# Kernel tuning notes

Measured on AMD Instinct MI355X. Metric: run time of the kernel, lower is better.

Reference implementation:

```python
import jax, jax.numpy as jnp
import numpy as np


def _box_iou(b1, b2):
    # torchvision.ops.box_iou: b1 [N,4], b2 [M,4] in (x1,y1,x2,y2) -> [N,M]
    area1 = (b1[:, 2] - b1[:, 0]) * (b1[:, 3] - b1[:, 1])
    area2 = (b2[:, 2] - b2[:, 0]) * (b2[:, 3] - b2[:, 1])
    lt = jnp.maximum(b1[:, None, :2], b2[None, :, :2])  # [N,M,2]
    rb = jnp.minimum(b1[:, None, 2:], b2[None, :, 2:])  # [N,M,2]
    wh = jnp.clip(rb - lt, 0.0)
    inter = wh[..., 0] * wh[..., 1]
    return inter / (area1[:, None] + area2[None, :] - inter)


def _hungarian_max(iou_np):
    # Maximize total IoU == minimize -IoU. iou_np: [N_pred, M_tgt], N >= M.
    # Classic O(n^2 m) shortest-augmenting-path Hungarian (host-side numpy;
    # the assignment is combinatorial and produces integer indices only).
    cost = -np.asarray(iou_np, dtype=np.float64).T  # [n=M_tgt, m=N_pred], n <= m
    n, m = cost.shape
    INF = 1e18
    u = np.zeros(n + 1)
    v = np.zeros(m + 1)
    p = np.zeros(m + 1, dtype=np.int64)   # p[j] = 1-based row matched to col j
    way = np.zeros(m + 1, dtype=np.int64)
    for i in range(1, n + 1):
        p[0] = i
        j0 = 0
        minv = np.full(m + 1, INF)
        used = np.zeros(m + 1, dtype=bool)
        while True:
            used[j0] = True
            i0 = p[j0]
            free = ~used[1:]
            cur = cost[i0 - 1, :] - u[i0] - v[1:]
            upd = free & (cur < minv[1:])
            mv = minv[1:]
            wy = way[1:]
            mv[upd] = cur[upd]
            wy[upd] = j0
            masked = np.where(free, mv, INF)
            j1 = int(np.argmin(masked)) + 1
            delta = masked[j1 - 1]
            u[p[used]] += delta
            v[used] -= delta
            mv[free] -= delta
            j0 = j1
            if p[j0] == 0:
                break
        while j0 != 0:
            j1 = way[j0]
            p[j0] = p[j1]
            j0 = j1
    row4col = p[1:]
    cols = np.nonzero(row4col > 0)[0]          # matched pred indices
    rows = row4col[cols] - 1                   # matched target indices
    return cols.astype(np.int64), rows.astype(np.int64)  # (matched_pred, matched_target)


def _make_boxes(kc, ks, shape):
    c = jax.random.uniform(kc, shape + (2,), dtype=jnp.float32)
    s = jax.random.uniform(ks, shape + (2,), dtype=jnp.float32) * 0.2 + 0.01
    return jnp.concatenate([c - s / 2, c + s / 2], axis=-1)


def setup_inputs() -> dict:
    key = jax.random.key(0)
    k1, k2, k3, k4, k5, k6 = jax.random.split(key, 6)
    N, C, B, K = 100000, 81, 16, 8
    result_boxes = _make_boxes(k1, k2, (N,))                      # [N,4] valid boxes
    result_confs = jax.random.normal(k3, (N, C), dtype=jnp.float32)
    target_locs = _make_boxes(k4, k5, (B, K))                     # [B,K,4]
    target_labels = jax.random.randint(k6, (B, K), 0, C, dtype=jnp.int64)
    return {
        "result_boxes": result_boxes,
        "result_confs": result_confs,
        "target_locs": target_locs,
        "target_labels": target_labels,
    }


def reference(result_boxes, result_confs, target_locs, target_labels):
    # Concatenating per-image targets == flattening batch dim
    total_locs = target_locs.reshape(-1, 4)        # [M,4]
    total_labels = target_labels.reshape(-1)       # [M]

    iou = _box_iou(result_boxes, total_locs)       # [N,M]
    matched_pred, matched_target = _hungarian_max(iou)
    mp = jnp.asarray(matched_pred)
    mt = jnp.asarray(matched_target)

    # SmoothL1 (beta=1, reduction='mean' over the 4 coords), summed over pairs
    d = result_boxes[mp] - total_locs[mt]          # [M,4]
    ad = jnp.abs(d)
    sl1 = jnp.where(ad < 1.0, 0.5 * d * d, ad - 0.5)
    reg_loss = jnp.sum(jnp.mean(sl1, axis=-1))

    # CrossEntropy per single (unbatched) sample, summed over pairs
    logits = result_confs[mp]                      # [M,C]
    labels = total_labels[mt]                      # [M]
    logp = jax.nn.log_softmax(logits, axis=-1)
    cls_loss = -jnp.sum(jnp.take_along_axis(logp, labels[:, None], axis=-1))

    train_acc = jnp.sum((jnp.argmax(logits, axis=-1) == labels).astype(jnp.int64))
    return (reg_loss + cls_loss, train_acc)
```

## Files before the change

kernel.cpp:

```cpp
#include <hip/hip_runtime.h>
#include <cstdint>
#include <cstddef>

typedef unsigned long long u64;
typedef unsigned int u32;

#define SLICES 2
#define SCAND 192
#define CAND 384
#define NSLOT 6
#define NBINS 4096
#define SEL_THR 1024
#define SEL_TARGET 128
#define POOLCAP 4096
#define MASKW 3200
#define TOP8 8

__device__ __forceinline__ float iou_f32(float4 p, float4 t, float area_t) {
  float area1 = (p.z - p.x) * (p.w - p.y);
  float ltx = fmaxf(p.x, t.x);
  float lty = fmaxf(p.y, t.y);
  float rbx = fminf(p.z, t.z);
  float rby = fminf(p.w, t.w);
  float wx = fmaxf(rbx - ltx, 0.0f);
  float wy = fmaxf(rby - lty, 0.0f);
  float inter = wx * wy;
  return inter / (area1 + area_t - inter);
}

__device__ __forceinline__ u64 map_cost(double cur) {
  u64 b = (u64)__double_as_longlong(cur);
  if (b == 0x8000000000000000ull) b = 0;
  return (b >> 63) ? ~b : (b | 0x8000000000000000ull);
}
__device__ __forceinline__ double unmap_cost(u64 m) {
  u64 b = (m >> 63) ? (m ^ 0x8000000000000000ull) : ~m;
  return __longlong_as_double((long long)b);
}


__global__ __launch_bounds__(SEL_THR) void select_kernel(const float4* __restrict__ pbox,
                                                         const float4* __restrict__ tbox,
                                                         u64* __restrict__ ckey,
                                                         int M, int NROWS) {
  __shared__ u32 s_hist[NBINS];
  __shared__ int s_csum[SEL_THR];
  __shared__ u64 s_pool[POOLCAP];
  __shared__ int s_n, s_n2, s_B;
  const int tid = threadIdx.x;
  const int lane = tid & 63;
  const int slice = blockIdx.x, row = blockIdx.y;
  const int sw = (M + SLICES - 1) / SLICES;
  const int base = slice * sw;
  const int send = min(base + sw, M);
  const float4 tb = tbox[row];
  const float area_t = (tb.z - tb.x) * (tb.w - tb.y);
  u64* orow_key = ckey + (size_t)row * CAND + slice * SCAND;

  for (int b = tid; b < NBINS; b += SEL_THR) s_hist[b] = 0;
  if (tid == 0) { s_n = 0; s_n2 = 0; s_B = 0; }
  __syncthreads();

  const u64 lowmask = (1ull << lane) - 1ull;
  const int iters = (sw + SEL_THR - 1) / SEL_THR;
  for (int it = 0; it < iters; ++it) {
    int j = base + it * SEL_THR + tid;
    bool inr = (j < send);
    float io = -1.0f;
    if (inr) io = iou_f32(pbox[j], tb, area_t);
    bool pos = inr && (io > 0.0f);
    u64 pm = __ballot(pos);
    int wn = (int)__popcll(pm);
    if (wn) {
      int wb = 0;
      if (lane == 0) wb = atomicAdd(&s_n, wn);
      wb = __shfl(wb, 0);
      if (pos) {
        int idx = wb + (int)__popcll(pm & lowmask);
        if (idx < POOLCAP) s_pool[idx] = ((u64)__float_as_uint(io) << 32) | (u64)(0xFFFFFFFFu - (u32)j);
        atomicAdd(&s_hist[__float_as_uint(io) >> 18], 1u);
      }
    }
  }
  __syncthreads();
  const int np = s_n;

  {
    int b0 = tid * 4;
    s_csum[tid] = (int)(s_hist[b0] + s_hist[b0 + 1] + s_hist[b0 + 2] + s_hist[b0 + 3]);
  }
  __syncthreads();

  if (tid < 64) {
    if (np >= SEL_TARGET) {
      int R = 0; bool found = false;
      for (int ch = SEL_THR / 64 - 1; ch >= 0 && !found; --ch) {
        int cum = s_csum[ch * 64 + tid];
        for (int off = 1; off < 64; off <<= 1) {
          int o = __shfl_down(cum, off);
          if (tid + off < 64) cum += o;
        }
        int chunksum = __shfl(cum, 0);
        if (R + chunksum >= SEL_TARGET) {
          u64 m = __ballot(R + cum >= SEL_TARGET);
          int l = 63 - __clzll(m);
          int R2 = R + ((l < 63) ? __shfl(cum, l + 1) : 0);
          if (tid == 0) {
            int bb = (ch * 64 + l) * 4;
            int B2 = bb;
            for (int b = bb + 3; b >= bb; --b) {
              R2 += (int)s_hist[b];
              if (R2 >= SEL_TARGET) { B2 = b; break; }
            }
            s_B = B2;
          }
          found = true;
        } else R += chunksum;
      }
    }
  }
  __syncthreads();
  const int B = s_B;

  if (np >= SEL_TARGET) {
    if (np <= POOLCAP) {
      for (int t = tid; t < np; t += SEL_THR) {
        u64 k = s_pool[t];
        if ((u32)(k >> 50) >= (u32)B) {
          int pos = atomicAdd(&s_n2, 1);
          if (pos < SCAND) orow_key[pos] = k;
        }
      }
    } else {
      for (int j = base + tid; j < send; j += SEL_THR) {
        float io = iou_f32(pbox[j], tb, area_t);
        if (io > 0.0f && (int)(__float_as_uint(io) >> 18) >= B) {
          int pos = atomicAdd(&s_n2, 1);
          if (pos < SCAND) orow_key[pos] = ((u64)__float_as_uint(io) << 32) | (u64)(0xFFFFFFFFu - (u32)j);
        }
      }
    }
    __syncthreads();
  } else {
    for (int t = tid; t < np; t += SEL_THR) {
      u64 k = s_pool[t];
      int pos = atomicAdd(&s_n2, 1);
      if (pos < SCAND) orow_key[pos] = k;
    }
    __syncthreads();
    if (tid < 64) {
      int need = SEL_TARGET - np, got = 0;
      int base_n = s_n2;
      for (int b2 = base; b2 < send && got < need; b2 += 64) {
        int j = b2 + tid;
        float io = (j < send) ? iou_f32(pbox[j], tb, area_t) : -1.0f;
        bool z = (j < send) && (io == 0.0f);
        u64 zm = __ballot(z);
        int rank = (int)__popcll(zm & ((1ull << tid) - 1ull));
        if (z && rank < need - got) {
          int pos = base_n + got + rank;
          if (pos < SCAND) orow_key[pos] = (u64)(0xFFFFFFFFu - (u32)j);
        }
        int zn = (int)__popcll(zm); if (zn > need - got) zn = need - got;
        got += zn;
      }
      if (tid == 0) s_n2 = base_n + got;
    }
    __syncthreads();
  }
  int n = min(s_n2, SCAND);
  for (int t2 = n + tid; t2 < SCAND; t2 += SEL_THR) orow_key[t2] = 0ull;
}

#define DPP_STEP(CTRL) do { \
  u32 ohi = (u32)__builtin_amdgcn_update_dpp((int)0xFFFFFFFF, (int)khi, (CTRL), 0xF, 0xF, false); \
  u32 olo = (u32)__builtin_amdgcn_update_dpp((int)0xFFFFFFFF, (int)klo, (CTRL), 0xF, 0xF, false); \
  int ocl =      __builtin_amdgcn_update_dpp((int)0x7FFFFFFF, kcol,     (CTRL), 0xF, 0xF, false); \
  bool lt = (ohi < khi) || (ohi == khi && ((olo < klo) || (olo == klo && ocl < kcol))); \
  if (lt) { khi = ohi; klo = olo; kcol = ocl; } \
} while (0)

#define DPPMAX(CTRL) do { \
  u32 oh2 = (u32)__builtin_amdgcn_update_dpp(0, (int)mhi, (CTRL), 0xF, 0xF, false); \
  u32 ol2 = (u32)__builtin_amdgcn_update_dpp(0, (int)mlo, (CTRL), 0xF, 0xF, false); \
  bool gt = (oh2 > mhi) || (oh2 == mhi && ol2 > mlo); \
  if (gt) { mhi = oh2; mlo = ol2; } \
} while (0)

__global__ __launch_bounds__(64) void top8_kernel(const u64* __restrict__ ckey,
                                                  u64* __restrict__ top8g, int NROWS) {
  const int lane = threadIdx.x;
  const int row = blockIdx.x;
  const u64* kp = ckey + (size_t)row * CAND;
  u64 k[NSLOT];
#pragma unroll
  for (int s = 0; s < NSLOT; ++s) k[s] = kp[(s << 6) + lane];
  u64 out = 0;
  for (int r = 0; r < TOP8; ++r) {
    u64 lmax = 0;
#pragma unroll
    for (int s = 0; s < NSLOT; ++s) if (k[s] > lmax) lmax = k[s];
    u32 mhi = (u32)(lmax >> 32), mlo = (u32)lmax;
    DPPMAX(0x111); DPPMAX(0x112); DPPMAX(0x114); DPPMAX(0x118); DPPMAX(0x142); DPPMAX(0x143);
    u32 ghi = (u32)__builtin_amdgcn_readlane((int)mhi, 63);
    u32 glo = (u32)__builtin_amdgcn_readlane((int)mlo, 63);
    u64 g = ((u64)ghi << 32) | (u64)glo;
    if (lane == r) out = g;
#pragma unroll
    for (int s = 0; s < NSLOT; ++s) if (k[s] == g) k[s] = 0;
  }
  if (lane < TOP8) top8g[(size_t)row * TOP8 + lane] = out;
}

#define STAGE_EVAL(KARR) do { \
  u64 lmax = 0; \
  _Pragma("unroll") \
  for (int s = 0; s < NSLOT; ++s) { \
    u64 k = (KARR)[s]; \
    if (k) { \
      u32 cw = 0xFFFFFFFFu - (u32)k; \
      if ((s_mask[cw >> 5] >> (cw & 31u)) & 1u) k = 0; \
      if (k > lmax) lmax = k; \
    } \
  } \
  u32 mhi = (u32)(lmax >> 32), mlo = (u32)lmax; \
  DPPMAX(0x111); DPPMAX(0x112); DPPMAX(0x114); DPPMAX(0x118); DPPMAX(0x142); DPPMAX(0x143); \
  u32 ghi = (u32)__builtin_amdgcn_readlane((int)mhi, 63); \
  u32 glo = (u32)__builtin_amdgcn_readlane((int)mlo, 63); \
  head_key = ((u64)ghi << 32) | (u64)glo; \
} while (0)

#define STAGE_LDS(RR) do { \
  u64 k = 0; \
  if (lane < TOP8) { \
    k = s_top8[(RR) - 1][lane]; \
    u32 cw = 0xFFFFFFFFu - (u32)k; \
    if ((s_mask[cw >> 5] >> (cw & 31u)) & 1u) k = 0; \
  } \
  u32 mhi = (u32)(k >> 32), mlo = (u32)k; \
  DPPMAX(0x111); DPPMAX(0x112); DPPMAX(0x114); \
  u32 ghi = (u32)__builtin_amdgcn_readlane((int)mhi, 7); \
  u32 glo = (u32)__builtin_amdgcn_readlane((int)mlo, 7); \
  head_key = ((u64)ghi << 32) | (u64)glo; \
  if (head_key == 0) { \
    u64 ck[NSLOT]; \
    const u64* kp = ckey + (size_t)((RR) - 1) * CAND; \
    _Pragma("unroll") \
    for (int s = 0; s < NSLOT; ++s) ck[s] = kp[(s << 6) + lane]; \
    STAGE_EVAL(ck); \
  } \
} while (0)

#define RECOMP_IOU(I0) do { \
  float4 tbi = s_tb[(I0) - 1]; \
  float ati = s_ta[(I0) - 1]; \
  oi0 = iou_f32(ob0, tbi, ati); \
  oi1 = iou_f32(ob1, tbi, ati); \
} while (0)

__global__ __launch_bounds__(64, 1) void match_kernel(const float4* __restrict__ pbox,
                                                      const float4* __restrict__ tboxg,
                                                      const u64* __restrict__ ckey,
                                                      const u64* __restrict__ top8g,
                                                      int* __restrict__ pairs,
                                                      int M, int NROWS) {
  const int lane = threadIdx.x;
  __shared__ u32 s_mask[MASKW];
  __shared__ u64 s_top8[128][TOP8];
  __shared__ float4 s_tb[128];
  __shared__ float  s_ta[128];

  for (int i = lane; i < MASKW; i += 64) s_mask[i] = 0;
  for (int i = lane; i < NROWS; i += 64) {
    float4 t = tboxg[i];
    s_tb[i] = t;
    s_ta[i] = (t.z - t.x) * (t.w - t.y);
  }
  for (int i = lane; i < NROWS * TOP8; i += 64) s_top8[i >> 3][i & 7] = top8g[i];
  __syncthreads();

  float4 zf = make_float4(0.f, 0.f, 0.f, 0.f);
  double u_a = 0.0, u_b = 0.0;
  int f_a = 0, f_b = 0;
  int oc0 = -1, orow0 = 0, ovis0 = 0; double ov0 = 0.0; float4 ob0 = zf; float oi0 = 0.0f;
  int oc1 = -1, orow1 = 0, ovis1 = 0; double ov1 = 0.0; float4 ob1 = zf; float oi1 = 0.0f;
  int nown = 0;

  u64 head_key = 0;
  float4 hbox = zf;
  int row = 1, i0 = 1;
  double u_i0 = 0.0;

  STAGE_LDS(1);
  hbox = pbox[0xFFFFFFFFu - (u32)head_key];
  f_a = (lane == 0); f_b = 0;
  u_i0 = 0.0;

  for (int guard = 0; guard < 5000; ++guard) {
    if (head_key == 0) break;

    u32 bhi = 0xFFFFFFFFu, blo = 0xFFFFFFFFu; int bcol = 0x7fffffff; int bsl = 15;
    if (oc0 >= 0 && ovis0 != row) {
      double cur = ((-(double)oi0) - u_i0) - ov0;
      u64 mk = map_cost(cur);
      bhi = (u32)(mk >> 32); blo = (u32)mk; bcol = oc0; bsl = 6;
    }
    if (oc1 >= 0 && ovis1 != row) {
      double cur = ((-(double)oi1) - u_i0) - ov1;
      u64 mk = map_cost(cur);
      u32 hi = (u32)(mk >> 32), lo = (u32)mk;
      bool t = (hi < bhi) || (hi == bhi && ((lo < blo) || (lo == blo && oc1 < bcol)));
      if (t) { bhi = hi; blo = lo; bcol = oc1; bsl = 7; }
    }
    u32 khi = bhi, klo = blo; int kcol = bcol;
    DPP_STEP(0x111); DPP_STEP(0x112); DPP_STEP(0x114); DPP_STEP(0x118);
    DPP_STEP(0x142); DPP_STEP(0x143);
    u32 rhi = (u32)__builtin_amdgcn_readlane((int)khi, 63);
    u32 rlo = (u32)__builtin_amdgcn_readlane((int)klo, 63);
    int rcol = __builtin_amdgcn_readlane(kcol, 63);

    float hio = __uint_as_float((u32)(head_key >> 32));
    int hcol = (int)(0xFFFFFFFFu - (u32)head_key);
    double curh = (-(double)hio) - u_i0;
    u64 mh = map_cost(curh);
    u32 hhi = (u32)(mh >> 32), hlo = (u32)mh;
    bool head_wins = (hhi < rhi) || (hhi == rhi && ((hlo < rlo) || (hlo == rlo && hcol < rcol)));
    const double delta = unmap_cost(head_wins ? mh : (((u64)rhi << 32) | (u64)rlo));

    if (f_a) u_a += delta;
    if (f_b) u_b += delta;
    u_i0 += delta;
    if (oc0 >= 0 && ovis0 == row) ov0 -= delta;
    if (oc1 >= 0 && ovis1 == row) ov1 -= delta;

    if (head_wins) {
      if (lane == 0) {
        pairs[row - 1] = hcol;
        atomicOr(&s_mask[(u32)hcol >> 5], 1u << ((u32)hcol & 31u));
      }
      int ne = nown, nl = ne & 63, nh = ne >> 6;
      if (lane == nl) {
        if (nh == 0) { oc0 = hcol; orow0 = row; ovis0 = 0; ov0 = 0.0; ob0 = hbox; }
        else         { oc1 = hcol; orow1 = row; ovis1 = 0; ov1 = 0.0; ob1 = hbox; }
      }
      nown = ne + 1;
      if (row == NROWS) break;
      ++row; i0 = row;
      asm volatile("s_waitcnt lgkmcnt(0)" ::: "memory");
      STAGE_LDS(row);
      hbox = pbox[0xFFFFFFFFu - (u32)head_key];
      RECOMP_IOU(row);
      f_a = (lane == ((row - 1) & 63)) && (((row - 1) >> 6) == 0);
      f_b = (lane == ((row - 1) & 63)) && (((row - 1) >> 6) == 1);
      u_i0 = 0.0;
    } else {
      bool eq = (bhi == rhi) && (blo == rlo) && (bcol == rcol);
      u64 wm = __ballot(eq);
      int L = (int)__ffsll((long long)wm) - 1;
      L = __builtin_amdgcn_readfirstlane(L);
      int s_w = __builtin_amdgcn_readlane(bsl, L);
      int o = __builtin_amdgcn_readlane((s_w == 6) ? orow0 : orow1, L);
      o = __builtin_amdgcn_readfirstlane(o);
      if (lane == L) { if (s_w == 6) ovis0 = row; else ovis1 = row; }
      int ol = (o - 1) & 63, oh = (o - 1) >> 6;
      if (lane == ol) { if (oh == 0) f_a = 1; else f_b = 1; }
      double uo = oh ? u_b : u_a;
      int uhi2 = __builtin_amdgcn_readlane(__double2hiint(uo), ol);
      int ulo2 = __builtin_amdgcn_readlane(__double2loint(uo), ol);
      u_i0 = __hiloint2double(uhi2, ulo2);
      i0 = o;
      STAGE_LDS(o);
      hbox = pbox[0xFFFFFFFFu - (u32)head_key];
      RECOMP_IOU(o);
    }
  }
}

__global__ __launch_bounds__(256) void loss_kernel(const float4* __restrict__ pbox,
                                                   const float* __restrict__ confs,
                                                   const float4* __restrict__ tbox,
                                                   const int* __restrict__ tlab,
                                                   const int* __restrict__ pairs,
                                                   float* __restrict__ out,
                                                   int NROWS, int C) {
  const int tid = threadIdx.x;
  __shared__ float s_reg[256];
  __shared__ float s_cls[256];
  __shared__ int   s_acc[256];
  float reg = 0.0f, cls = 0.0f; int acc = 0;
  if (tid < NROWS) {
    int pred = pairs[tid];
    float4 pb = pbox[pred];
    float4 tb = tbox[tid];
    float d0 = pb.x - tb.x, d1 = pb.y - tb.y, d2 = pb.z - tb.z, d3 = pb.w - tb.w;
    float a0 = fabsf(d0), a1 = fabsf(d1), a2 = fabsf(d2), a3 = fabsf(d3);
    float s = 0.0f;
    s += (a0 < 1.0f) ? 0.5f * d0 * d0 : a0 - 0.5f;
    s += (a1 < 1.0f) ? 0.5f * d1 * d1 : a1 - 0.5f;
    s += (a2 < 1.0f) ? 0.5f * d2 * d2 : a2 - 0.5f;
    s += (a3 < 1.0f) ? 0.5f * d3 * d3 : a3 - 0.5f;
    reg = s * 0.25f;

    const float* lg = confs + (long long)pred * C;
    float mx = lg[0]; int am = 0;
    for (int k = 1; k < C; ++k) { float x = lg[k]; if (x > mx) { mx = x; am = k; } }
    double se = 0.0;
    for (int k = 0; k < C; ++k) se += exp((double)(lg[k] - mx));
    int lab = tlab[tid];
    double logp = (double)(lg[lab] - mx) - log(se);
    cls = (float)(-logp);
    acc = (am == lab) ? 1 : 0;
  }
  s_reg[tid] = reg; s_cls[tid] = cls; s_acc[tid] = acc;
  __syncthreads();
  for (int s2 = 128; s2 > 0; s2 >>= 1) {
    if (tid < s2) {
      s_reg[tid] += s_reg[tid + s2];
      s_cls[tid] += s_cls[tid + s2];
      s_acc[tid] += s_acc[tid + s2];
    }
    __syncthreads();
  }
  if (tid == 0) {
    out[0] = s_reg[0] + s_cls[0];
    out[1] = (float)s_acc[0];
  }
}

extern "C" void kernel_launch(void* const* d_in, const int* in_sizes, int n_in,
                              void* d_out, int out_size, void* d_ws, size_t ws_size,
                              hipStream_t stream) {
  const float4* pbox  = (const float4*)d_in[0];
  const float*  confs = (const float*)d_in[1];
  const float4* tbox  = (const float4*)d_in[2];
  const int*    tlab  = (const int*)d_in[3];

  int N = in_sizes[0] / 4;
  int C = in_sizes[1] / N;
  int NROWS = in_sizes[2] / 4;
  int M = N;

  char* w = (char*)d_ws;
  auto alloc = [&](size_t sz) { char* r = w; w += (sz + 255) & ~(size_t)255; return r; };
  u64* ckey  = (u64*)alloc((size_t)NROWS * CAND * sizeof(u64));
  u64* top8g = (u64*)alloc((size_t)NROWS * TOP8 * sizeof(u64));
  int* pairs = (int*)alloc((size_t)(NROWS + 8) * sizeof(int));

  select_kernel<<<dim3(SLICES, NROWS), SEL_THR, 0, stream>>>(pbox, tbox, ckey, M, NROWS);
  top8_kernel<<<NROWS, 64, 0, stream>>>(ckey, top8g, NROWS);
  match_kernel<<<1, 64, 0, stream>>>(pbox, tbox, ckey, top8g, pairs, M, NROWS);
  loss_kernel<<<1, 256, 0, stream>>>(pbox, confs, tbox, tlab, pairs,
                                     (float*)d_out, NROWS, C);
}
```

Measured before the change: 251.2 us.

## Add fast-path bound check to skip owned-column scan and keep top8 in registers

The match loop keeps a running bound (vmax) on owned-column potentials. When the head candidate's reduced cost provably beats every owned column, it augments directly and skips the IoU recompute and the wave-wide DPP min-reduction. Per-row top-8 candidates and target boxes now live in registers, fetched with readlane and a select tree, instead of LDS. This trades LDS traffic and the per-step reduction for more register pressure and a correctness-critical bound argument.

Result: slower. 279.3 us (+11.2%).

```diff
diff --git a/kernel.cpp b/kernel.cpp
--- a/kernel.cpp
+++ b/kernel.cpp
@@ -212,51 +212,23 @@
   if (lane < TOP8) top8g[(size_t)row * TOP8 + lane] = out;
 }
 
-#define STAGE_EVAL(KARR) do { \
-  u64 lmax = 0; \
-  _Pragma("unroll") \
-  for (int s = 0; s < NSLOT; ++s) { \
-    u64 k = (KARR)[s]; \
-    if (k) { \
-      u32 cw = 0xFFFFFFFFu - (u32)k; \
-      if ((s_mask[cw >> 5] >> (cw & 31u)) & 1u) k = 0; \
-      if (k > lmax) lmax = k; \
-    } \
-  } \
-  u32 mhi = (u32)(lmax >> 32), mlo = (u32)lmax; \
-  DPPMAX(0x111); DPPMAX(0x112); DPPMAX(0x114); DPPMAX(0x118); DPPMAX(0x142); DPPMAX(0x143); \
-  u32 ghi = (u32)__builtin_amdgcn_readlane((int)mhi, 63); \
-  u32 glo = (u32)__builtin_amdgcn_readlane((int)mlo, 63); \
-  head_key = ((u64)ghi << 32) | (u64)glo; \
-} while (0)
-
-#define STAGE_LDS(RR) do { \
-  u64 k = 0; \
-  if (lane < TOP8) { \
-    k = s_top8[(RR) - 1][lane]; \
-    u32 cw = 0xFFFFFFFFu - (u32)k; \
-    if ((s_mask[cw >> 5] >> (cw & 31u)) & 1u) k = 0; \
-  } \
-  u32 mhi = (u32)(k >> 32), mlo = (u32)k; \
-  DPPMAX(0x111); DPPMAX(0x112); DPPMAX(0x114); \
-  u32 ghi = (u32)__builtin_amdgcn_readlane((int)mhi, 7); \
-  u32 glo = (u32)__builtin_amdgcn_readlane((int)mlo, 7); \
-  head_key = ((u64)ghi << 32) | (u64)glo; \
-  if (head_key == 0) { \
-    u64 ck[NSLOT]; \
-    const u64* kp = ckey + (size_t)((RR) - 1) * CAND; \
-    _Pragma("unroll") \
-    for (int s = 0; s < NSLOT; ++s) ck[s] = kp[(s << 6) + lane]; \
-    STAGE_EVAL(ck); \
-  } \
-} while (0)
-
-#define RECOMP_IOU(I0) do { \
-  float4 tbi = s_tb[(I0) - 1]; \
-  float ati = s_ta[(I0) - 1]; \
-  oi0 = iou_f32(ob0, tbi, ati); \
-  oi1 = iou_f32(ob1, tbi, ati); \
-} while (0)
+__device__ __forceinline__ u64 sel16(const u64* t8, int ri) {
+  u64 a0 = (ri & 1) ? t8[1]  : t8[0];
+  u64 a1 = (ri & 1) ? t8[3]  : t8[2];
+  u64 a2 = (ri & 1) ? t8[5]  : t8[4];
+  u64 a3 = (ri & 1) ? t8[7]  : t8[6];
+  u64 a4 = (ri & 1) ? t8[9]  : t8[8];
+  u64 a5 = (ri & 1) ? t8[11] : t8[10];
+  u64 a6 = (ri & 1) ? t8[13] : t8[12];
+  u64 a7 = (ri & 1) ? t8[15] : t8[14];
+  u64 b0 = (ri & 2) ? a1 : a0;
+  u64 b1 = (ri & 2) ? a3 : a2;
+  u64 b2 = (ri & 2) ? a5 : a4;
+  u64 b3 = (ri & 2) ? a7 : a6;
+  u64 c0 = (ri & 4) ? b1 : b0;
+  u64 c1 = (ri & 4) ? b3 : b2;
+  return (ri & 8) ? c1 : c0;
+}
 
 __global__ __launch_bounds__(64, 1) void match_kernel(const float4* __restrict__ pbox,
                                                       const float4* __restrict__ tboxg,
@@ -266,112 +238,190 @@
                                                       int M, int NROWS) {
   const int lane = threadIdx.x;
   __shared__ u32 s_mask[MASKW];
-  __shared__ u64 s_top8[128][TOP8];
-  __shared__ float4 s_tb[128];
-  __shared__ float  s_ta[128];
-
   for (int i = lane; i < MASKW; i += 64) s_mask[i] = 0;
-  for (int i = lane; i < NROWS; i += 64) {
-    float4 t = tboxg[i];
-    s_tb[i] = t;
-    s_ta[i] = (t.z - t.x) * (t.w - t.y);
-  }
-  for (int i = lane; i < NROWS * TOP8; i += 64) s_top8[i >> 3][i & 7] = top8g[i];
   __syncthreads();
 
   float4 zf = make_float4(0.f, 0.f, 0.f, 0.f);
+  float4 tbA = (lane < NROWS) ? tboxg[lane] : zf;
+  float4 tbB = (lane + 64 < NROWS) ? tboxg[lane + 64] : zf;
+
+  u64 t8[16];
+#pragma unroll
+  for (int r = 0; r < 16; ++r) {
+    int rw = (lane >> 3) + (r << 3);
+    t8[r] = (rw < NROWS) ? top8g[(size_t)rw * TOP8 + (lane & 7)] : 0ull;
+  }
+
   double u_a = 0.0, u_b = 0.0;
   int f_a = 0, f_b = 0;
-  int oc0 = -1, orow0 = 0, ovis0 = 0; double ov0 = 0.0; float4 ob0 = zf; float oi0 = 0.0f;
-  int oc1 = -1, orow1 = 0, ovis1 = 0; double ov1 = 0.0; float4 ob1 = zf; float oi1 = 0.0f;
+  int oc0 = -1, orow0 = 0, ovis0 = 0; double ov0 = 0.0; float4 ob0 = zf;
+  int oc1 = -1, orow1 = 0, ovis1 = 0; double ov1 = 0.0; float4 ob1 = zf;
   int nown = 0;
+  double vmax = 0.0;
+  bool inchain = false;
 
   u64 head_key = 0;
   float4 hbox = zf;
   int row = 1, i0 = 1;
   double u_i0 = 0.0;
 
-  STAGE_LDS(1);
+  auto stage_reg = [&](int rr) -> u64 {
+    int rr0 = rr - 1;
+    u64 sel = sel16(t8, rr0 >> 3);
+    int g = rr0 & 7;
+    if ((lane >> 3) != g) sel = 0;
+    u32 mhi = (u32)(sel >> 32), mlo = (u32)sel;
+    DPPMAX(0x111); DPPMAX(0x112); DPPMAX(0x114);
+    u32 ghi = (u32)__builtin_amdgcn_readlane((int)mhi, (g << 3) + 7);
+    u32 glo = (u32)__builtin_amdgcn_readlane((int)mlo, (g << 3) + 7);
+    u64 hk = ((u64)ghi << 32) | (u64)glo;
+    if (hk == 0) {
+      asm volatile("s_waitcnt lgkmcnt(0)" ::: "memory");
+      const u64* kp = ckey + (size_t)rr0 * CAND;
+      u64 lmax = 0;
+#pragma unroll
+      for (int s = 0; s < NSLOT; ++s) {
+        u64 k = kp[(s << 6) + lane];
+        if (k) {
+          u32 cw = 0xFFFFFFFFu - (u32)k;
+          if ((s_mask[cw >> 5] >> (cw & 31u)) & 1u) k = 0;
+          if (k > lmax) lmax = k;
+        }
+      }
+      u32 mh2 = (u32)(lmax >> 32), ml2 = (u32)lmax;
+      { u32 mhi = mh2, mlo = ml2;
+        DPPMAX(0x111); DPPMAX(0x112); DPPMAX(0x114); DPPMAX(0x118); DPPMAX(0x142); DPPMAX(0x143);
+        mh2 = (u32)__builtin_amdgcn_readlane((int)mhi, 63);
+        ml2 = (u32)__builtin_amdgcn_readlane((int)mlo, 63); }
+      hk = ((u64)mh2 << 32) | (u64)ml2;
+    }
+    return hk;
+  };
+
+  head_key = stage_reg(1);
   hbox = pbox[0xFFFFFFFFu - (u32)head_key];
   f_a = (lane == 0); f_b = 0;
   u_i0 = 0.0;
 
-  for (int guard = 0; guard < 5000; ++guard) {
+  bool fin = false;
+  for (int guard = 0; guard < 5000 && !fin; ++guard) {
     if (head_key == 0) break;
-
-    u32 bhi = 0xFFFFFFFFu, blo = 0xFFFFFFFFu; int bcol = 0x7fffffff; int bsl = 15;
-    if (oc0 >= 0 && ovis0 != row) {
-      double cur = ((-(double)oi0) - u_i0) - ov0;
-      u64 mk = map_cost(cur);
-      bhi = (u32)(mk >> 32); blo = (u32)mk; bcol = oc0; bsl = 6;
-    }
-    if (oc1 >= 0 && ovis1 != row) {
-      double cur = ((-(double)oi1) - u_i0) - ov1;
-      u64 mk = map_cost(cur);
-      u32 hi = (u32)(mk >> 32), lo = (u32)mk;
-      bool t = (hi < bhi) || (hi == bhi && ((lo < blo) || (lo == blo && oc1 < bcol)));
-      if (t) { bhi = hi; blo = lo; bcol = oc1; bsl = 7; }
-    }
-    u32 khi = bhi, klo = blo; int kcol = bcol;
-    DPP_STEP(0x111); DPP_STEP(0x112); DPP_STEP(0x114); DPP_STEP(0x118);
-    DPP_STEP(0x142); DPP_STEP(0x143);
-    u32 rhi = (u32)__builtin_amdgcn_readlane((int)khi, 63);
-    u32 rlo = (u32)__builtin_amdgcn_readlane((int)klo, 63);
-    int rcol = __builtin_amdgcn_readlane(kcol, 63);
 
     float hio = __uint_as_float((u32)(head_key >> 32));
     int hcol = (int)(0xFFFFFFFFu - (u32)head_key);
     double curh = (-(double)hio) - u_i0;
-    u64 mh = map_cost(curh);
-    u32 hhi = (u32)(mh >> 32), hlo = (u32)mh;
-    bool head_wins = (hhi < rhi) || (hhi == rhi && ((hlo < rlo) || (hlo == rlo && hcol < rcol)));
-    const double delta = unmap_cost(head_wins ? mh : (((u64)rhi << 32) | (u64)rlo));
+
+    bool fast;
+    if (nown == 0) fast = true;
+    else {
+      double bound = (-1.0 - u_i0) - vmax;
+      fast = (bound > curh);
+    }
+
+    double delta;
+    bool do_aug;
+    int jc = hcol;
+
+    if (fast) {
+      delta = curh;
+      do_aug = true;
+    } else {
+      int li = (i0 - 1) & 63, hb2 = (i0 - 1) >> 6;
+      float tx = __int_as_float(__builtin_amdgcn_readlane(__float_as_int(hb2 ? tbB.x : tbA.x), li));
+      float ty = __int_as_float(__builtin_amdgcn_readlane(__float_as_int(hb2 ? tbB.y : tbA.y), li));
+      float tz = __int_as_float(__builtin_amdgcn_readlane(__float_as_int(hb2 ? tbB.z : tbA.z), li));
+      float tw = __int_as_float(__builtin_amdgcn_readlane(__float_as_int(hb2 ? tbB.w : tbA.w), li));
+      float4 tbi = make_float4(tx, ty, tz, tw);
+      float ati = (tz - tx) * (tw - ty);
+
+      u32 bhi = 0xFFFFFFFFu, blo = 0xFFFFFFFFu; int bcol = 0x7fffffff; int bsl = 15;
+      if (oc0 >= 0 && ovis0 != row) {
+        float io2 = iou_f32(ob0, tbi, ati);
+        double cur = ((-(double)io2) - u_i0) - ov0;
+        u64 mk = map_cost(cur);
+        bhi = (u32)(mk >> 32); blo = (u32)mk; bcol = oc0; bsl = 6;
+      }
+      if (oc1 >= 0 && ovis1 != row) {
+        float io2 = iou_f32(ob1, tbi, ati);
+        double cur = ((-(double)io2) - u_i0) - ov1;
+        u64 mk = map_cost(cur);
+        u32 hi = (u32)(mk >> 32), lo = (u32)mk;
+        bool t = (hi < bhi) || (hi == bhi && ((lo < blo) || (lo == blo && oc1 < bcol)));
+        if (t) { bhi = hi; blo = lo; bcol = oc1; bsl = 7; }
+      }
+      u32 khi = bhi, klo = blo; int kcol = bcol;
+      DPP_STEP(0x111); DPP_STEP(0x112); DPP_STEP(0x114); DPP_STEP(0x118);
+      DPP_STEP(0x142); DPP_STEP(0x143);
+      u32 rhi = (u32)__builtin_amdgcn_readlane((int)khi, 63);
+      u32 rlo = (u32)__builtin_amdgcn_readlane((int)klo, 63);
+      int rcol = __builtin_amdgcn_readlane(kcol, 63);
+
+      u64 mh = map_cost(curh);
+      u32 hhi = (u32)(mh >> 32), hlo = (u32)mh;
+      bool head_wins = (hhi < rhi) || (hhi == rhi && ((hlo < rlo) || (hlo == rlo && hcol < rcol)));
+      delta = unmap_cost(head_wins ? mh : (((u64)rhi << 32) | (u64)rlo));
+      do_aug = head_wins;
+
+      if (!head_wins) {
+        bool eq = (bhi == rhi) && (blo == rlo) && (bcol == rcol);
+        u64 wm = __ballot(eq);
+        int L = (int)__ffsll((long long)wm) - 1;
+        L = __builtin_amdgcn_readfirstlane(L);
+        int s_w = __builtin_amdgcn_readlane(bsl, L);
+        int o = __builtin_amdgcn_readlane((s_w == 6) ? orow0 : orow1, L);
+        o = __builtin_amdgcn_readfirstlane(o);
+        if (f_a) u_a += delta;
+        if (f_b) u_b += delta;
+        u_i0 += delta;
+        if (oc0 >= 0 && ovis0 == row) ov0 -= delta;
+        if (oc1 >= 0 && ovis1 == row) ov1 -= delta;
+        if (inchain) vmax = fmax(vmax, vmax - delta);
+        inchain = true;
+        if (lane == L) { if (s_w == 6) ovis0 = row; else ovis1 = row; }
+        int ol = (o - 1) & 63, oh = (o - 1) >> 6;
+        if (lane == ol) { if (oh == 0) f_a = 1; else f_b = 1; }
+        double uo = oh ? u_b : u_a;
+        int uhi2 = __builtin_amdgcn_readlane(__double2hiint(uo), ol);
+        int ulo2 = __builtin_amdgcn_readlane(__double2loint(uo), ol);
+        u_i0 = __hiloint2double(uhi2, ulo2);
+        i0 = o;
+        head_key = stage_reg(o);
+        hbox = pbox[0xFFFFFFFFu - (u32)head_key];
+        continue;
+      }
+    }
 
     if (f_a) u_a += delta;
     if (f_b) u_b += delta;
-    u_i0 += delta;
     if (oc0 >= 0 && ovis0 == row) ov0 -= delta;
     if (oc1 >= 0 && ovis1 == row) ov1 -= delta;
-
-    if (head_wins) {
-      if (lane == 0) {
-        pairs[row - 1] = hcol;
-        atomicOr(&s_mask[(u32)hcol >> 5], 1u << ((u32)hcol & 31u));
-      }
+    if (inchain) vmax = fmax(vmax, vmax - delta);
+
+    if (lane == 0) {
+      pairs[row - 1] = jc;
+      atomicOr(&s_mask[(u32)jc >> 5], 1u << ((u32)jc & 31u));
+    }
+    {
+      u32 cjw = 0xFFFFFFFFu - (u32)jc;
+#pragma unroll
+      for (int r = 0; r < 16; ++r) if ((u32)t8[r] == cjw) t8[r] = 0;
+    }
+    {
       int ne = nown, nl = ne & 63, nh = ne >> 6;
       if (lane == nl) {
-        if (nh == 0) { oc0 = hcol; orow0 = row; ovis0 = 0; ov0 = 0.0; ob0 = hbox; }
-        else         { oc1 = hcol; orow1 = row; ovis1 = 0; ov1 = 0.0; ob1 = hbox; }
+        if (nh == 0) { oc0 = jc; orow0 = row; ovis0 = 0; ov0 = 0.0; ob0 = hbox; }
+        else         { oc1 = jc; orow1 = row; ovis1 = 0; ov1 = 0.0; ob1 = hbox; }
       }
       nown = ne + 1;
-      if (row == NROWS) break;
-      ++row; i0 = row;
-      asm volatile("s_waitcnt lgkmcnt(0)" ::: "memory");
-      STAGE_LDS(row);
-      hbox = pbox[0xFFFFFFFFu - (u32)head_key];
-      RECOMP_IOU(row);
+    }
+    vmax = fmax(vmax, 0.0);
+    if (row == NROWS) { fin = true; }
+    else {
+      ++row; i0 = row; u_i0 = 0.0; inchain = false;
       f_a = (lane == ((row - 1) & 63)) && (((row - 1) >> 6) == 0);
       f_b = (lane == ((row - 1) & 63)) && (((row - 1) >> 6) == 1);
-      u_i0 = 0.0;
-    } else {
-      bool eq = (bhi == rhi) && (blo == rlo) && (bcol == rcol);
-      u64 wm = __ballot(eq);
-      int L = (int)__ffsll((long long)wm) - 1;
-      L = __builtin_amdgcn_readfirstlane(L);
-      int s_w = __builtin_amdgcn_readlane(bsl, L);
-      int o = __builtin_amdgcn_readlane((s_w == 6) ? orow0 : orow1, L);
-      o = __builtin_amdgcn_readfirstlane(o);
-      if (lane == L) { if (s_w == 6) ovis0 = row; else ovis1 = row; }
-      int ol = (o - 1) & 63, oh = (o - 1) >> 6;
-      if (lane == ol) { if (oh == 0) f_a = 1; else f_b = 1; }
-      double uo = oh ? u_b : u_a;
-      int uhi2 = __builtin_amdgcn_readlane(__double2hiint(uo), ol);
-      int ulo2 = __builtin_amdgcn_readlane(__double2loint(uo), ol);
-      u_i0 = __hiloint2double(uhi2, ulo2);
-      i0 = o;
-      STAGE_LDS(o);
+      head_key = stage_reg(row);
       hbox = pbox[0xFFFFFFFFu - (u32)head_key];
-      RECOMP_IOU(o);
     }
   }
 }
```

## Fuse loss into match kernel and precompute top-8 boxes to shorten serial chain

Applied to the files above, without the earlier changes.

The top8 kernel now also gathers the prediction boxes for each row's top-8 candidates, so the serial Hungarian loop takes the head box from LDS via a lane readlane instead of a dependent global load. When a row finishes, the next row's head is taken from the top two candidates already prefetched, and IoU is recomputed on the fly from target boxes held in registers. The loss kernel is folded into the match kernel (256 threads, one wave runs the matching), which removes a launch and the global pairs buffer. This adds LDS and register pressure and makes the serial loop's control flow more complex.

After: 279.8 us. 1.11x slower.

```diff
diff --git a/kernel.cpp b/kernel.cpp
--- a/kernel.cpp
+++ b/kernel.cpp
@@ -187,8 +187,10 @@
   if (gt) { mhi = oh2; mlo = ol2; } \
 } while (0)
 
-__global__ __launch_bounds__(64) void top8_kernel(const u64* __restrict__ ckey,
-                                                  u64* __restrict__ top8g, int NROWS) {
+__global__ __launch_bounds__(64) void top8_kernel(const float4* __restrict__ pbox,
+                                                  const u64* __restrict__ ckey,
+                                                  u64* __restrict__ top8g,
+                                                  float4* __restrict__ top8b, int NROWS) {
   const int lane = threadIdx.x;
   const int row = blockIdx.x;
   const u64* kp = ckey + (size_t)row * CAND;
@@ -209,189 +211,221 @@
 #pragma unroll
     for (int s = 0; s < NSLOT; ++s) if (k[s] == g) k[s] = 0;
   }
-  if (lane < TOP8) top8g[(size_t)row * TOP8 + lane] = out;
-}
-
-#define STAGE_EVAL(KARR) do { \
-  u64 lmax = 0; \
-  _Pragma("unroll") \
-  for (int s = 0; s < NSLOT; ++s) { \
-    u64 k = (KARR)[s]; \
-    if (k) { \
-      u32 cw = 0xFFFFFFFFu - (u32)k; \
-      if ((s_mask[cw >> 5] >> (cw & 31u)) & 1u) k = 0; \
-      if (k > lmax) lmax = k; \
-    } \
+  if (lane < TOP8) {
+    top8g[(size_t)row * TOP8 + lane] = out;
+    int col = (int)(0xFFFFFFFFu - (u32)out);
+    top8b[(size_t)row * TOP8 + lane] = out ? pbox[col] : make_float4(0.f, 0.f, 0.f, 0.f);
+  }
+}
+
+#define RDLF(X, L) __int_as_float(__builtin_amdgcn_readlane(__float_as_int(X), (L)))
+
+#define COLD_STAGE(RR) do { \
+  u64 kk = 0; float4 kb = zf; \
+  if (lane < TOP8) { \
+    kk = s_t8[((RR) - 1) * TOP8 + lane]; \
+    kb = s_t8b[((RR) - 1) * TOP8 + lane]; \
+    u32 cw = 0xFFFFFFFFu - (u32)kk; \
+    if (kk && ((s_mask[cw >> 5] >> (cw & 31u)) & 1u)) kk = 0; \
   } \
-  u32 mhi = (u32)(lmax >> 32), mlo = (u32)lmax; \
-  DPPMAX(0x111); DPPMAX(0x112); DPPMAX(0x114); DPPMAX(0x118); DPPMAX(0x142); DPPMAX(0x143); \
-  u32 ghi = (u32)__builtin_amdgcn_readlane((int)mhi, 63); \
-  u32 glo = (u32)__builtin_amdgcn_readlane((int)mlo, 63); \
-  head_key = ((u64)ghi << 32) | (u64)glo; \
-} while (0)
-
-#define STAGE_LDS(RR) do { \
-  u64 k = 0; \
-  if (lane < TOP8) { \
-    k = s_top8[(RR) - 1][lane]; \
-    u32 cw = 0xFFFFFFFFu - (u32)k; \
-    if ((s_mask[cw >> 5] >> (cw & 31u)) & 1u) k = 0; \
-  } \
-  u32 mhi = (u32)(k >> 32), mlo = (u32)k; \
+  u32 mhi = (u32)(kk >> 32), mlo = (u32)kk; \
   DPPMAX(0x111); DPPMAX(0x112); DPPMAX(0x114); \
   u32 ghi = (u32)__builtin_amdgcn_readlane((int)mhi, 7); \
   u32 glo = (u32)__builtin_amdgcn_readlane((int)mlo, 7); \
   head_key = ((u64)ghi << 32) | (u64)glo; \
-  if (head_key == 0) { \
-    u64 ck[NSLOT]; \
-    const u64* kp = ckey + (size_t)((RR) - 1) * CAND; \
+  if (head_key != 0) { \
+    int eL = (int)__ffsll((long long)__ballot(kk == head_key && kk != 0)) - 1; \
+    eL = __builtin_amdgcn_readfirstlane(eL); \
+    hbox.x = RDLF(kb.x, eL); hbox.y = RDLF(kb.y, eL); \
+    hbox.z = RDLF(kb.z, eL); hbox.w = RDLF(kb.w, eL); \
+  } else { \
+    const u64* kp2 = ckey + (size_t)((RR) - 1) * CAND; \
+    u64 lmax = 0; \
     _Pragma("unroll") \
-    for (int s = 0; s < NSLOT; ++s) ck[s] = kp[(s << 6) + lane]; \
-    STAGE_EVAL(ck); \
+    for (int s = 0; s < NSLOT; ++s) { \
+      u64 kf = kp2[(s << 6) + lane]; \
+      if (kf) { \
+        u32 cw = 0xFFFFFFFFu - (u32)kf; \
+        if ((s_mask[cw >> 5] >> (cw & 31u)) & 1u) kf = 0; \
+        if (kf > lmax) lmax = kf; \
+      } \
+    } \
+    u32 m2hi = (u32)(lmax >> 32), m2lo = (u32)lmax; \
+    { u32 mhi = m2hi, mlo = m2lo; \
+      DPPMAX(0x111); DPPMAX(0x112); DPPMAX(0x114); DPPMAX(0x118); DPPMAX(0x142); DPPMAX(0x143); \
+      m2hi = (u32)__builtin_amdgcn_readlane((int)mhi, 63); \
+      m2lo = (u32)__builtin_amdgcn_readlane((int)mlo, 63); } \
+    head_key = ((u64)m2hi << 32) | (u64)m2lo; \
+    if (head_key) hbox = pbox[0xFFFFFFFFu - (u32)head_key]; \
   } \
 } while (0)
 
-#define RECOMP_IOU(I0) do { \
-  float4 tbi = s_tb[(I0) - 1]; \
-  float ati = s_ta[(I0) - 1]; \
-  oi0 = iou_f32(ob0, tbi, ati); \
-  oi1 = iou_f32(ob1, tbi, ati); \
-} while (0)
-
-__global__ __launch_bounds__(64, 1) void match_kernel(const float4* __restrict__ pbox,
-                                                      const float4* __restrict__ tboxg,
-                                                      const u64* __restrict__ ckey,
-                                                      const u64* __restrict__ top8g,
-                                                      int* __restrict__ pairs,
-                                                      int M, int NROWS) {
-  const int lane = threadIdx.x;
+__global__ __launch_bounds__(256, 1) void match_kernel(const float4* __restrict__ pbox,
+                                                       const float4* __restrict__ tboxg,
+                                                       const u64* __restrict__ ckey,
+                                                       const u64* __restrict__ top8g,
+                                                       const float4* __restrict__ top8b,
+                                                       const float* __restrict__ confs,
+                                                       const int* __restrict__ tlab,
+                                                       float* __restrict__ out,
+                                                       int M, int NROWS, int C) {
+  const int tid = threadIdx.x;
+  const int lane = tid & 63;
+  const int wv = tid >> 6;
   __shared__ u32 s_mask[MASKW];
-  __shared__ u64 s_top8[128][TOP8];
-  __shared__ float4 s_tb[128];
-  __shared__ float  s_ta[128];
-
-  for (int i = lane; i < MASKW; i += 64) s_mask[i] = 0;
-  for (int i = lane; i < NROWS; i += 64) {
-    float4 t = tboxg[i];
-    s_tb[i] = t;
-    s_ta[i] = (t.z - t.x) * (t.w - t.y);
-  }
-  for (int i = lane; i < NROWS * TOP8; i += 64) s_top8[i >> 3][i & 7] = top8g[i];
-  __syncthreads();
-
-  float4 zf = make_float4(0.f, 0.f, 0.f, 0.f);
-  double u_a = 0.0, u_b = 0.0;
-  int f_a = 0, f_b = 0;
-  int oc0 = -1, orow0 = 0, ovis0 = 0; double ov0 = 0.0; float4 ob0 = zf; float oi0 = 0.0f;
-  int oc1 = -1, orow1 = 0, ovis1 = 0; double ov1 = 0.0; float4 ob1 = zf; float oi1 = 0.0f;
-  int nown = 0;
-
-  u64 head_key = 0;
-  float4 hbox = zf;
-  int row = 1, i0 = 1;
-  double u_i0 = 0.0;
-
-  STAGE_LDS(1);
-  hbox = pbox[0xFFFFFFFFu - (u32)head_key];
-  f_a = (lane == 0); f_b = 0;
-  u_i0 = 0.0;
-
-  for (int guard = 0; guard < 5000; ++guard) {
-    if (head_key == 0) break;
-
-    u32 bhi = 0xFFFFFFFFu, blo = 0xFFFFFFFFu; int bcol = 0x7fffffff; int bsl = 15;
-    if (oc0 >= 0 && ovis0 != row) {
-      double cur = ((-(double)oi0) - u_i0) - ov0;
-      u64 mk = map_cost(cur);
-      bhi = (u32)(mk >> 32); blo = (u32)mk; bcol = oc0; bsl = 6;
-    }
-    if (oc1 >= 0 && ovis1 != row) {
-      double cur = ((-(double)oi1) - u_i0) - ov1;
-      u64 mk = map_cost(cur);
-      u32 hi = (u32)(mk >> 32), lo = (u32)mk;
-      bool t = (hi < bhi) || (hi == bhi && ((lo < blo) || (lo == blo && oc1 < bcol)));
-      if (t) { bhi = hi; blo = lo; bcol = oc1; bsl = 7; }
-    }
-    u32 khi = bhi, klo = blo; int kcol = bcol;
-    DPP_STEP(0x111); DPP_STEP(0x112); DPP_STEP(0x114); DPP_STEP(0x118);
-    DPP_STEP(0x142); DPP_STEP(0x143);
-    u32 rhi = (u32)__builtin_amdgcn_readlane((int)khi, 63);
-    u32 rlo = (u32)__builtin_amdgcn_readlane((int)klo, 63);
-    int rcol = __builtin_amdgcn_readlane(kcol, 63);
-
-    float hio = __uint_as_float((u32)(head_key >> 32));
-    int hcol = (int)(0xFFFFFFFFu - (u32)head_key);
-    double curh = (-(double)hio) - u_i0;
-    u64 mh = map_cost(curh);
-    u32 hhi = (u32)(mh >> 32), hlo = (u32)mh;
-    bool head_wins = (hhi < rhi) || (hhi == rhi && ((hlo < rlo) || (hlo == rlo && hcol < rcol)));
-    const double delta = unmap_cost(head_wins ? mh : (((u64)rhi << 32) | (u64)rlo));
-
-    if (f_a) u_a += delta;
-    if (f_b) u_b += delta;
-    u_i0 += delta;
-    if (oc0 >= 0 && ovis0 == row) ov0 -= delta;
-    if (oc1 >= 0 && ovis1 == row) ov1 -= delta;
-
-    if (head_wins) {
-      if (lane == 0) {
-        pairs[row - 1] = hcol;
-        atomicOr(&s_mask[(u32)hcol >> 5], 1u << ((u32)hcol & 31u));
-      }
-      int ne = nown, nl = ne & 63, nh = ne >> 6;
-      if (lane == nl) {
-        if (nh == 0) { oc0 = hcol; orow0 = row; ovis0 = 0; ov0 = 0.0; ob0 = hbox; }
-        else         { oc1 = hcol; orow1 = row; ovis1 = 0; ov1 = 0.0; ob1 = hbox; }
-      }
-      nown = ne + 1;
-      if (row == NROWS) break;
-      ++row; i0 = row;
-      asm volatile("s_waitcnt lgkmcnt(0)" ::: "memory");
-      STAGE_LDS(row);
-      hbox = pbox[0xFFFFFFFFu - (u32)head_key];
-      RECOMP_IOU(row);
-      f_a = (lane == ((row - 1) & 63)) && (((row - 1) >> 6) == 0);
-      f_b = (lane == ((row - 1) & 63)) && (((row - 1) >> 6) == 1);
-      u_i0 = 0.0;
-    } else {
-      bool eq = (bhi == rhi) && (blo == rlo) && (bcol == rcol);
-      u64 wm = __ballot(eq);
-      int L = (int)__ffsll((long long)wm) - 1;
-      L = __builtin_amdgcn_readfirstlane(L);
-      int s_w = __builtin_amdgcn_readlane(bsl, L);
-      int o = __builtin_amdgcn_readlane((s_w == 6) ? orow0 : orow1, L);
-      o = __builtin_amdgcn_readfirstlane(o);
-      if (lane == L) { if (s_w == 6) ovis0 = row; else ovis1 = row; }
-      int ol = (o - 1) & 63, oh = (o - 1) >> 6;
-      if (lane == ol) { if (oh == 0) f_a = 1; else f_b = 1; }
-      double uo = oh ? u_b : u_a;
-      int uhi2 = __builtin_amdgcn_readlane(__double2hiint(uo), ol);
-      int ulo2 = __builtin_amdgcn_readlane(__double2loint(uo), ol);
-      u_i0 = __hiloint2double(uhi2, ulo2);
-      i0 = o;
-      STAGE_LDS(o);
-      hbox = pbox[0xFFFFFFFFu - (u32)head_key];
-      RECOMP_IOU(o);
-    }
-  }
-}
-
-__global__ __launch_bounds__(256) void loss_kernel(const float4* __restrict__ pbox,
-                                                   const float* __restrict__ confs,
-                                                   const float4* __restrict__ tbox,
-                                                   const int* __restrict__ tlab,
-                                                   const int* __restrict__ pairs,
-                                                   float* __restrict__ out,
-                                                   int NROWS, int C) {
-  const int tid = threadIdx.x;
+  __shared__ u64 s_t8[128 * TOP8];
+  __shared__ float4 s_t8b[128 * TOP8];
+  __shared__ int s_pairs[128];
   __shared__ float s_reg[256];
   __shared__ float s_cls[256];
   __shared__ int   s_acc[256];
+
+  for (int i = tid; i < MASKW; i += 256) s_mask[i] = 0;
+  for (int i = tid; i < NROWS * TOP8; i += 256) { s_t8[i] = top8g[i]; s_t8b[i] = top8b[i]; }
+  __syncthreads();
+
+  if (wv == 0) {
+    float4 zf = make_float4(0.f, 0.f, 0.f, 0.f);
+    float4 tbA = (lane < NROWS) ? tboxg[lane] : zf;
+    float4 tbB = (lane + 64 < NROWS) ? tboxg[lane + 64] : zf;
+
+    double u_a = 0.0, u_b = 0.0;
+    int f_a = 0, f_b = 0;
+    int oc0 = -1, orow0 = 0, ovis0 = 0; double ov0 = 0.0; float4 ob0 = zf;
+    int oc1 = -1, orow1 = 0, ovis1 = 0; double ov1 = 0.0; float4 ob1 = zf;
+    int nown = 0;
+    u64 head_key = 0; float4 hbox = zf;
+    int row = 1, i0 = 1;
+    double u_i0 = 0.0;
+
+    COLD_STAGE(1);
+    f_a = (lane == 0); f_b = 0;
+
+    for (int guard = 0; guard < 5000; ++guard) {
+      if (head_key == 0) break;
+
+      int sr0 = (row < NROWS) ? row : NROWS - 1;
+      u64 sk = 0; float4 sbox = zf;
+      if (lane < TOP8) {
+        sk = s_t8[sr0 * TOP8 + lane];
+        sbox = s_t8b[sr0 * TOP8 + lane];
+        u32 cw = 0xFFFFFFFFu - (u32)sk;
+        if (sk && ((s_mask[cw >> 5] >> (cw & 31u)) & 1u)) sk = 0;
+      }
+
+      int li = (i0 - 1) & 63, hb2 = (i0 - 1) >> 6;
+      float tx = RDLF(hb2 ? tbB.x : tbA.x, li);
+      float ty = RDLF(hb2 ? tbB.y : tbA.y, li);
+      float tz = RDLF(hb2 ? tbB.z : tbA.z, li);
+      float tw = RDLF(hb2 ? tbB.w : tbA.w, li);
+      float4 tbi = make_float4(tx, ty, tz, tw);
+      float ati = (tz - tx) * (tw - ty);
+
+      u32 bhi = 0xFFFFFFFFu, blo = 0xFFFFFFFFu; int bcol = 0x7fffffff; int bsl = 15;
+      if (oc0 >= 0 && ovis0 != row) {
+        float io2 = iou_f32(ob0, tbi, ati);
+        double cur = ((-(double)io2) - u_i0) - ov0;
+        u64 mk = map_cost(cur);
+        bhi = (u32)(mk >> 32); blo = (u32)mk; bcol = oc0; bsl = 6;
+      }
+      if (oc1 >= 0 && ovis1 != row) {
+        float io2 = iou_f32(ob1, tbi, ati);
+        double cur = ((-(double)io2) - u_i0) - ov1;
+        u64 mk = map_cost(cur);
+        u32 hi = (u32)(mk >> 32), lo = (u32)mk;
+        bool t = (hi < bhi) || (hi == bhi && ((lo < blo) || (lo == blo && oc1 < bcol)));
+        if (t) { bhi = hi; blo = lo; bcol = oc1; bsl = 7; }
+      }
+      u32 khi = bhi, klo = blo; int kcol = bcol;
+      DPP_STEP(0x111); DPP_STEP(0x112); DPP_STEP(0x114); DPP_STEP(0x118);
+      DPP_STEP(0x142); DPP_STEP(0x143);
+      u32 rhi = (u32)__builtin_amdgcn_readlane((int)khi, 63);
+      u32 rlo = (u32)__builtin_amdgcn_readlane((int)klo, 63);
+      int rcol = __builtin_amdgcn_readlane(kcol, 63);
+
+      float hio = __uint_as_float((u32)(head_key >> 32));
+      int hcol = (int)(0xFFFFFFFFu - (u32)head_key);
+      double curh = (-(double)hio) - u_i0;
+      u64 mh = map_cost(curh);
+      u32 hhi = (u32)(mh >> 32), hlo = (u32)mh;
+      bool head_wins = (hhi < rhi) || (hhi == rhi && ((hlo < rlo) || (hlo == rlo && hcol < rcol)));
+      const double delta = unmap_cost(head_wins ? mh : (((u64)rhi << 32) | (u64)rlo));
+
+      if (f_a) u_a += delta;
+      if (f_b) u_b += delta;
+      u_i0 += delta;
+      if (oc0 >= 0 && ovis0 == row) ov0 -= delta;
+      if (oc1 >= 0 && ovis1 == row) ov1 -= delta;
+
+      if (head_wins) {
+        const int jc = hcol;
+        u64 k1, k2;
+        { u32 mhi = (u32)(sk >> 32), mlo = (u32)sk;
+          DPPMAX(0x111); DPPMAX(0x112); DPPMAX(0x114);
+          k1 = ((u64)(u32)__builtin_amdgcn_readlane((int)mhi, 7) << 32) |
+               (u64)(u32)__builtin_amdgcn_readlane((int)mlo, 7); }
+        u64 skz = (sk == k1) ? 0 : sk;
+        { u32 mhi = (u32)(skz >> 32), mlo = (u32)skz;
+          DPPMAX(0x111); DPPMAX(0x112); DPPMAX(0x114);
+          k2 = ((u64)(u32)__builtin_amdgcn_readlane((int)mhi, 7) << 32) |
+               (u64)(u32)__builtin_amdgcn_readlane((int)mlo, 7); }
+        int e1 = (int)__ffsll((long long)__ballot(sk == k1 && sk != 0)) - 1;
+        int e2 = (int)__ffsll((long long)__ballot(skz == k2 && skz != 0)) - 1;
+        e1 = __builtin_amdgcn_readfirstlane(e1);
+        e2 = __builtin_amdgcn_readfirstlane(e2);
+        float4 b1 = zf, b2 = zf;
+        if (e1 >= 0) { b1.x = RDLF(sbox.x, e1); b1.y = RDLF(sbox.y, e1);
+                       b1.z = RDLF(sbox.z, e1); b1.w = RDLF(sbox.w, e1); }
+        if (e2 >= 0) { b2.x = RDLF(sbox.x, e2); b2.y = RDLF(sbox.y, e2);
+                       b2.z = RDLF(sbox.z, e2); b2.w = RDLF(sbox.w, e2); }
+
+        if (lane == 0) {
+          s_pairs[row - 1] = jc;
+          atomicOr(&s_mask[(u32)jc >> 5], 1u << ((u32)jc & 31u));
+        }
+        {
+          int ne = nown, nl = ne & 63, nh = ne >> 6;
+          if (lane == nl) {
+            if (nh == 0) { oc0 = jc; orow0 = row; ovis0 = 0; ov0 = 0.0; ob0 = hbox; }
+            else         { oc1 = jc; orow1 = row; ovis1 = 0; ov1 = 0.0; ob1 = hbox; }
+          }
+          nown = ne + 1;
+        }
+        if (row == NROWS) break;
+        ++row; i0 = row; u_i0 = 0.0;
+        f_a = (lane == ((row - 1) & 63)) && (((row - 1) >> 6) == 0);
+        f_b = (lane == ((row - 1) & 63)) && (((row - 1) >> 6) == 1);
+        u32 jw = 0xFFFFFFFFu - (u32)jc;
+        if ((u32)k1 == jw && k1 != 0) { head_key = k2; hbox = b2; }
+        else                          { head_key = k1; hbox = b1; }
+        if (head_key == 0) { COLD_STAGE(row); }
+      } else {
+        bool eq = (bhi == rhi) && (blo == rlo) && (bcol == rcol);
+        u64 wm = __ballot(eq);
+        int L = (int)__ffsll((long long)wm) - 1;
+        L = __builtin_amdgcn_readfirstlane(L);
+        int s_w = __builtin_amdgcn_readlane(bsl, L);
+        int o = __builtin_amdgcn_readlane((s_w == 6) ? orow0 : orow1, L);
+        o = __builtin_amdgcn_readfirstlane(o);
+        if (lane == L) { if (s_w == 6) ovis0 = row; else ovis1 = row; }
+        int ol = (o - 1) & 63, oh = (o - 1) >> 6;
+        if (lane == ol) { if (oh == 0) f_a = 1; else f_b = 1; }
+        double uo = oh ? u_b : u_a;
+        int uhi2 = __builtin_amdgcn_readlane(__double2hiint(uo), ol);
+        int ulo2 = __builtin_amdgcn_readlane(__double2loint(uo), ol);
+        u_i0 = __hiloint2double(uhi2, ulo2);
+        i0 = o;
+        COLD_STAGE(o);
+      }
+    }
+  }
+  __syncthreads();
+
   float reg = 0.0f, cls = 0.0f; int acc = 0;
   if (tid < NROWS) {
-    int pred = pairs[tid];
+    int pred = s_pairs[tid];
     float4 pb = pbox[pred];
-    float4 tb = tbox[tid];
+    float4 tb = tboxg[tid];
     float d0 = pb.x - tb.x, d1 = pb.y - tb.y, d2 = pb.z - tb.z, d3 = pb.w - tb.w;
     float a0 = fabsf(d0), a1 = fabsf(d1), a2 = fabsf(d2), a3 = fabsf(d3);
     float s = 0.0f;
@@ -442,13 +476,12 @@
 
   char* w = (char*)d_ws;
   auto alloc = [&](size_t sz) { char* r = w; w += (sz + 255) & ~(size_t)255; return r; };
-  u64* ckey  = (u64*)alloc((size_t)NROWS * CAND * sizeof(u64));
-  u64* top8g = (u64*)alloc((size_t)NROWS * TOP8 * sizeof(u64));
-  int* pairs = (int*)alloc((size_t)(NROWS + 8) * sizeof(int));
+  u64*    ckey  = (u64*)   alloc((size_t)NROWS * CAND * sizeof(u64));
+  u64*    top8g = (u64*)   alloc((size_t)NROWS * TOP8 * sizeof(u64));
+  float4* top8b = (float4*)alloc((size_t)NROWS * TOP8 * sizeof(float4));
 
   select_kernel<<<dim3(SLICES, NROWS), SEL_THR, 0, stream>>>(pbox, tbox, ckey, M, NROWS);
-  top8_kernel<<<NROWS, 64, 0, stream>>>(ckey, top8g, NROWS);
-  match_kernel<<<1, 64, 0, stream>>>(pbox, tbox, ckey, top8g, pairs, M, NROWS);
-  loss_kernel<<<1, 256, 0, stream>>>(pbox, confs, tbox, tlab, pairs,
-                                     (float*)d_out, NROWS, C);
-}
+  top8_kernel<<<NROWS, 64, 0, stream>>>(pbox, ckey, top8g, top8b, NROWS);
+  match_kernel<<<1, 256, 0, stream>>>(pbox, tbox, ckey, top8g, top8b,
+                                      confs, tlab, (float*)d_out, M, NROWS, C);
+}
```
